# Kernel tuning notes

Hardware: AMD Instinct MI355X
Metric: run time of the kernel (lower is better)

The kernel has to match this reference:

```python
import jax, jax.numpy as jnp
import numpy as np

B, D = 64, 512          # batch, in_dims
P, PS, S = 128, 3, 64   # num_patches, patch_size, scene_size


def setup_inputs() -> dict:
    key = jax.random.key(0)
    k0, k1, k2, k3 = jax.random.split(key, 4)
    z = jax.random.normal(k0, (B, D), jnp.float32)
    Wm = jax.random.normal(k1, (P * PS * PS, D), jnp.float32) * 0.02
    bm = jnp.zeros((P * PS * PS,), jnp.float32)
    Wt = jax.random.normal(k2, (6 * P, D), jnp.float32) * 0.01
    # module initializes transform bias to [scale,0,0,0,scale,0] per patch (scale=2)
    bt = jnp.tile(jnp.array([2.0, 0.0, 0.0, 0.0, 2.0, 0.0], jnp.float32), P)
    noise = jax.random.normal(k3, (PS, PS), jnp.float32)
    return {"z": z, "Wm": Wm, "bm": bm, "Wt": Wt, "bt": bt, "noise": noise}


def _affine_grid(theta, size):
    # theta: (N,2,3). Matches torch affine_grid(align_corners=False).
    c = (jnp.arange(size, dtype=theta.dtype) + 0.5) / size * 2.0 - 1.0
    xg, yg = jnp.meshgrid(c, c)  # xg[h,w]=c[w], yg[h,w]=c[h]
    base = jnp.stack([xg, yg, jnp.ones_like(xg)], axis=-1)  # (S,S,3)
    return jnp.einsum('nij,hwj->nhwi', theta, base)  # (N,S,S,2), [...,0]=x, [...,1]=y


def _grid_sample_bilinear_zeros(img, grid):
    # img: (N,Hi,Wi), grid: (N,Ho,Wo,2). torch grid_sample bilinear, zeros padding,
    # align_corners=False.
    N, Hi, Wi = img.shape
    ix = ((grid[..., 0] + 1.0) * Wi - 1.0) * 0.5
    iy = ((grid[..., 1] + 1.0) * Hi - 1.0) * 0.5
    ix0 = jnp.floor(ix)
    iy0 = jnp.floor(iy)
    wx1 = ix - ix0
    wy1 = iy - iy0
    wx0 = 1.0 - wx1
    wy0 = 1.0 - wy1
    b = jnp.arange(N)[:, None, None]

    def gather(xf, yf):
        xi = xf.astype(jnp.int32)
        yi = yf.astype(jnp.int32)
        valid = (xi >= 0) & (xi < Wi) & (yi >= 0) & (yi < Hi)
        xc = jnp.clip(xi, 0, Wi - 1)
        yc = jnp.clip(yi, 0, Hi - 1)
        return jnp.where(valid, img[b, yc, xc], 0.0)

    v00 = gather(ix0, iy0)
    v01 = gather(ix0 + 1.0, iy0)
    v10 = gather(ix0, iy0 + 1.0)
    v11 = gather(ix0 + 1.0, iy0 + 1.0)
    return (wy0 * (wx0 * v00 + wx1 * v01) + wy1 * (wx0 * v10 + wx1 * v11))


def reference(z, Wm, bm, Wt, bt, noise):
    Bz = z.shape[0]
    # refine_patches=True path: masks = 1 - sigmoid(Linear(z))
    masks = 1.0 - jax.nn.sigmoid(z @ Wm.T + bm)
    masks = masks.reshape(Bz, P, PS, PS) * noise  # patch_noise multiply
    theta = (z @ Wt.T + bt).reshape(Bz, P, 2, 3)
    imgs = masks.reshape(Bz * P, PS, PS)
    th = theta.reshape(Bz * P, 2, 3)
    grid = _affine_grid(th, S)                      # (B*P, S, S, 2)
    out = _grid_sample_bilinear_zeros(imgs, grid)   # (B*P, S, S)
    return out.reshape(Bz, P, S, S)
```

## Files before the change

### kernel.cpp

```cpp
#include <hip/hip_runtime.h>
#include <math.h>

#define BATCH 64
#define DIM 512
#define NPATCH 128
#define SSZ 64
#define PADZ 516

typedef float f32x4 __attribute__((ext_vector_type(4)));

__global__ __launch_bounds__(256) void k_gemm(
    const float* __restrict__ z, const float* __restrict__ Wm,
    const float* __restrict__ bm, const float* __restrict__ Wt,
    const float* __restrict__ bt, const float* __restrict__ noise,
    float* __restrict__ ws) {
  __shared__ float zs[16 * PADZ];
  const int p = blockIdx.x;
  const int bq = blockIdx.y;
  const int t = threadIdx.x;

  {
    const f32x4* __restrict__ src = (const f32x4*)(z + (size_t)(bq * 16) * DIM);
#pragma unroll
    for (int i = 0; i < 8; ++i) {
      const int idx = t + (i << 8);
      const int row = idx >> 7;
      const int col = idx & 127;
      *(f32x4*)(zs + row * PADZ + (col << 2)) = src[idx];
    }
  }
  __syncthreads();

  const int r = t >> 4;
  const int bl = t & 15;
  if (r >= 15) return;

  const float* __restrict__ wrow =
      (r < 9) ? (Wm + (size_t)(p * 9 + r) * DIM)
              : (Wt + (size_t)(p * 6 + (r - 9)) * DIM);
  const float* __restrict__ zr = zs + bl * PADZ;

  float a0 = 0.0f, a1 = 0.0f, a2 = 0.0f, a3 = 0.0f;
#pragma unroll 8
  for (int i = 0; i < 128; ++i) {
    const f32x4 wv = ((const f32x4*)wrow)[i];
    const f32x4 zv = *(const f32x4*)(zr + (i << 2));
    a0 = fmaf(wv.x, zv.x, a0);
    a1 = fmaf(wv.y, zv.y, a1);
    a2 = fmaf(wv.z, zv.z, a2);
    a3 = fmaf(wv.w, zv.w, a3);
  }
  const float acc = (a0 + a1) + (a2 + a3);

  const int b = (bq << 4) + bl;
  float v;
  if (r < 9) {
    v = (1.0f / (1.0f + expf(acc + bm[p * 9 + r]))) * noise[r];
  } else {
    v = acc + bt[p * 6 + (r - 9)];
  }
  ws[(((size_t)b << 7) + p) * 16 + r] = v;
}

__global__ __launch_bounds__(256) void k_sample(
    const float* __restrict__ ws, float* __restrict__ out) {
  __shared__ float sm[16];
  const int t = threadIdx.x;
  const int bp = blockIdx.x;
  if (t < 16) sm[t] = ws[((size_t)bp << 4) + t];
  __syncthreads();

  const float m00 = sm[0], m01 = sm[1], m02 = sm[2];
  const float m10 = sm[3], m11 = sm[4], m12 = sm[5];
  const float m20 = sm[6], m21 = sm[7], m22 = sm[8];
  const float th0 = sm[9], th1 = sm[10], th2 = sm[11];
  const float th3 = sm[12], th4 = sm[13], th5 = sm[14];

  const int w4 = (t & 15) << 2;
  const int hb = t >> 4;
  const float cx0 = (w4 + 0.5f) * (1.0f / 32.0f) - 1.0f;
  const float cy0 = (hb + 0.5f) * (1.0f / 32.0f) - 1.0f;
  const float dix = th0 * (1.5f / 32.0f);
  const float diy = th3 * (1.5f / 32.0f);
  const float Bx = 1.5f * th1, By = 1.5f * th4;
  const float Px = fmaf(1.5f, fmaf(th0, cx0, th2), 1.0f);
  const float Py = fmaf(1.5f, fmaf(th3, cx0, th5), 1.0f);

  float* op = out + ((size_t)bp << 12) + hb * 64 + w4;

#pragma unroll
  for (int i = 0; i < 4; ++i) {
    const float cy = cy0 + 0.5f * i;
    const float ix = fmaf(Bx, cy, Px);
    const float iy = fmaf(By, cy, Py);
    float ax = ix + 1.0f, bx = 1.0f - ix;
    float ay = iy + 1.0f, by = 1.0f - iy;
    f32x4 rv;
#pragma unroll
    for (int j = 0; j < 4; ++j) {
      const float wx0 = __builtin_amdgcn_fmed3f(0.0f, ax, bx);
      const float wx1 = __builtin_amdgcn_fmed3f(0.0f, ax - 1.0f, bx + 1.0f);
      const float wx2 = __builtin_amdgcn_fmed3f(0.0f, ax - 2.0f, bx + 2.0f);
      const float wy0 = __builtin_amdgcn_fmed3f(0.0f, ay, by);
      const float wy1 = __builtin_amdgcn_fmed3f(0.0f, ay - 1.0f, by + 1.0f);
      const float wy2 = __builtin_amdgcn_fmed3f(0.0f, ay - 2.0f, by + 2.0f);
      const float s0 = fmaf(m02, wx2, fmaf(m01, wx1, m00 * wx0));
      const float s1 = fmaf(m12, wx2, fmaf(m11, wx1, m10 * wx0));
      const float s2 = fmaf(m22, wx2, fmaf(m21, wx1, m20 * wx0));
      rv[j] = fmaf(wy2, s2, fmaf(wy1, s1, wy0 * s0));
      ax += dix; bx -= dix;
      ay += diy; by -= diy;
    }
    __builtin_nontemporal_store(rv, (f32x4*)(op + i * 16 * 64));
  }
}

__global__ __launch_bounds__(256) void k_fused(
    const float* __restrict__ z, const float* __restrict__ Wm,
    const float* __restrict__ bm, const float* __restrict__ Wt,
    const float* __restrict__ bt, const float* __restrict__ noise,
    float* __restrict__ out) {
  __shared__ float sm[16];

  const int t = threadIdx.x;
  const int bp = blockIdx.x;
  const int b = bp >> 7;
  const int p = bp & 127;

  const int r = t >> 4;
  const int c = t & 15;
  float acc = 0.0f;
  if (r < 15) {
    const float* __restrict__ wrow =
        (r < 9) ? (Wm + (size_t)(p * 9 + r) * DIM)
                : (Wt + (size_t)(p * 6 + (r - 9)) * DIM);
    const float* __restrict__ zrow = z + (size_t)b * DIM;
#pragma unroll
    for (int i = 0; i < 8; ++i) {
      const float4 wv = *(const float4*)(wrow + i * 64 + c * 4);
      const float4 zv = *(const float4*)(zrow + i * 64 + c * 4);
      acc = fmaf(wv.x, zv.x, acc);
      acc = fmaf(wv.y, zv.y, acc);
      acc = fmaf(wv.z, zv.z, acc);
      acc = fmaf(wv.w, zv.w, acc);
    }
  }
  acc += __shfl_xor(acc, 1);
  acc += __shfl_xor(acc, 2);
  acc += __shfl_xor(acc, 4);
  acc += __shfl_xor(acc, 8);
  if (c == 0 && r < 15) {
    float v = acc;
    if (r < 9) {
      v = (1.0f / (1.0f + expf(v + bm[p * 9 + r]))) * noise[r];
    } else {
      v += bt[p * 6 + (r - 9)];
    }
    sm[r] = v;
  }
  __syncthreads();

  const float m00 = sm[0], m01 = sm[1], m02 = sm[2];
  const float m10 = sm[3], m11 = sm[4], m12 = sm[5];
  const float m20 = sm[6], m21 = sm[7], m22 = sm[8];
  const float th0 = sm[9], th1 = sm[10], th2 = sm[11];
  const float th3 = sm[12], th4 = sm[13], th5 = sm[14];

  const int w4 = (t & 15) << 2;
  const int hb = t >> 4;
  const float cx0 = (w4 + 0.5f) * (1.0f / 32.0f) - 1.0f;
  const float cy0 = (hb + 0.5f) * (1.0f / 32.0f) - 1.0f;
  const float dix = th0 * (1.5f / 32.0f);
  const float diy = th3 * (1.5f / 32.0f);
  const float Bx = 1.5f * th1, By = 1.5f * th4;
  const float Px = fmaf(1.5f, fmaf(th0, cx0, th2), 1.0f);
  const float Py = fmaf(1.5f, fmaf(th3, cx0, th5), 1.0f);

  float* op = out + ((size_t)bp << 12) + hb * 64 + w4;

#pragma unroll
  for (int i = 0; i < 4; ++i) {
    const float cy = cy0 + 0.5f * i;
    float ix = fmaf(Bx, cy, Px);
    float iy = fmaf(By, cy, Py);
    float4 rv;
    float* rp = &rv.x;
#pragma unroll
    for (int j = 0; j < 4; ++j) {
      const float wx0 = fmaxf(1.0f - fabsf(ix), 0.0f);
      const float wx1 = fmaxf(1.0f - fabsf(ix - 1.0f), 0.0f);
      const float wx2 = fmaxf(1.0f - fabsf(ix - 2.0f), 0.0f);
      const float wy0 = fmaxf(1.0f - fabsf(iy), 0.0f);
      const float wy1 = fmaxf(1.0f - fabsf(iy - 1.0f), 0.0f);
      const float wy2 = fmaxf(1.0f - fabsf(iy - 2.0f), 0.0f);
      const float s0 = fmaf(m02, wx2, fmaf(m01, wx1, m00 * wx0));
      const float s1 = fmaf(m12, wx2, fmaf(m11, wx1, m10 * wx0));
      const float s2 = fmaf(m22, wx2, fmaf(m21, wx1, m20 * wx0));
      rp[j] = fmaf(wy2, s2, fmaf(wy1, s1, wy0 * s0));
      ix += dix;
      iy += diy;
    }
    *(float4*)(op + i * 16 * 64) = rv;
  }
}

extern "C" void kernel_launch(void* const* d_in, const int* in_sizes, int n_in,
                              void* d_out, int out_size, void* d_ws, size_t ws_size,
                              hipStream_t stream) {
  const float* z     = (const float*)d_in[0];
  const float* Wm    = (const float*)d_in[1];
  const float* bm    = (const float*)d_in[2];
  const float* Wt    = (const float*)d_in[3];
  const float* bt    = (const float*)d_in[4];
  const float* noise = (const float*)d_in[5];
  float* out = (float*)d_out;

  const size_t need = (size_t)BATCH * NPATCH * 16 * sizeof(float);
  if (d_ws != nullptr && ws_size >= need) {
    float* ws = (float*)d_ws;
    hipLaunchKernelGGL(k_gemm, dim3(NPATCH, 4), dim3(256), 0, stream,
                       z, Wm, bm, Wt, bt, noise, ws);
    hipLaunchKernelGGL(k_sample, dim3(BATCH * NPATCH), dim3(256), 0, stream,
                       ws, out);
  } else {
    hipLaunchKernelGGL(k_fused, dim3(BATCH * NPATCH), dim3(256), 0, stream,
                       z, Wm, bm, Wt, bt, noise, out);
  }
}
```

Measured before the change: 162.4 us.

## Assign one wavefront per patch in sampling kernel, broadcast params via shuffles

The sampling kernel now gives each 64-lane wavefront a whole 64x64 patch, so a 256-thread block covers four patches and the grid shrinks fourfold. Per-patch parameters are loaded by one lane each and broadcast with wave shuffles instead of going through shared memory and a block barrier. Each lane loops over 16 row groups and writes float4s with ordinary stores in place of nontemporal ones. This removes the shared-memory staging and __syncthreads, at the cost of more serial work per thread and a change in output caching behaviour.

```diff
diff --git a/kernel.cpp b/kernel.cpp
--- a/kernel.cpp
+++ b/kernel.cpp
@@ -64,40 +64,38 @@
 
 __global__ __launch_bounds__(256) void k_sample(
     const float* __restrict__ ws, float* __restrict__ out) {
-  __shared__ float sm[16];
-  const int t = threadIdx.x;
-  const int bp = blockIdx.x;
-  if (t < 16) sm[t] = ws[((size_t)bp << 4) + t];
-  __syncthreads();
-
-  const float m00 = sm[0], m01 = sm[1], m02 = sm[2];
-  const float m10 = sm[3], m11 = sm[4], m12 = sm[5];
-  const float m20 = sm[6], m21 = sm[7], m22 = sm[8];
-  const float th0 = sm[9], th1 = sm[10], th2 = sm[11];
-  const float th3 = sm[12], th4 = sm[13], th5 = sm[14];
-
-  const int w4 = (t & 15) << 2;
-  const int hb = t >> 4;
+  const int lane = threadIdx.x & 63;
+  const int bp = (blockIdx.x << 2) | (threadIdx.x >> 6);
+
+  const float rec = ws[((size_t)bp << 4) + (lane & 15)];
+  const float m00 = __shfl(rec, 0), m01 = __shfl(rec, 1), m02 = __shfl(rec, 2);
+  const float m10 = __shfl(rec, 3), m11 = __shfl(rec, 4), m12 = __shfl(rec, 5);
+  const float m20 = __shfl(rec, 6), m21 = __shfl(rec, 7), m22 = __shfl(rec, 8);
+  const float th0 = __shfl(rec, 9), th1 = __shfl(rec, 10), th2 = __shfl(rec, 11);
+  const float th3 = __shfl(rec, 12), th4 = __shfl(rec, 13), th5 = __shfl(rec, 14);
+
+  const int w4 = (lane & 15) << 2;
+  const int rsub = lane >> 4;
   const float cx0 = (w4 + 0.5f) * (1.0f / 32.0f) - 1.0f;
-  const float cy0 = (hb + 0.5f) * (1.0f / 32.0f) - 1.0f;
+  const float cy0 = (rsub + 0.5f) * (1.0f / 32.0f) - 1.0f;
   const float dix = th0 * (1.5f / 32.0f);
   const float diy = th3 * (1.5f / 32.0f);
-  const float Bx = 1.5f * th1, By = 1.5f * th4;
-  const float Px = fmaf(1.5f, fmaf(th0, cx0, th2), 1.0f);
-  const float Py = fmaf(1.5f, fmaf(th3, cx0, th5), 1.0f);
-
-  float* op = out + ((size_t)bp << 12) + hb * 64 + w4;
-
-#pragma unroll
-  for (int i = 0; i < 4; ++i) {
-    const float cy = cy0 + 0.5f * i;
-    const float ix = fmaf(Bx, cy, Px);
-    const float iy = fmaf(By, cy, Py);
-    float ax = ix + 1.0f, bx = 1.0f - ix;
-    float ay = iy + 1.0f, by = 1.0f - iy;
+  const float dAx = th1 * (1.5f * 0.125f);
+  const float dAy = th4 * (1.5f * 0.125f);
+  const float ixb0 = fmaf(1.5f, fmaf(th0, cx0, fmaf(th1, cy0, th2)), 1.0f);
+  const float iyb0 = fmaf(1.5f, fmaf(th3, cx0, fmaf(th4, cy0, th5)), 1.0f);
+
+  float* op = out + ((size_t)bp << 12) + (rsub << 6) + w4;
+
+#pragma unroll 2
+  for (int a = 0; a < 16; ++a) {
+    float ix = fmaf((float)a, dAx, ixb0);
+    float iy = fmaf((float)a, dAy, iyb0);
     f32x4 rv;
 #pragma unroll
     for (int j = 0; j < 4; ++j) {
+      const float ax = ix + 1.0f, bx = 1.0f - ix;
+      const float ay = iy + 1.0f, by = 1.0f - iy;
       const float wx0 = __builtin_amdgcn_fmed3f(0.0f, ax, bx);
       const float wx1 = __builtin_amdgcn_fmed3f(0.0f, ax - 1.0f, bx + 1.0f);
       const float wx2 = __builtin_amdgcn_fmed3f(0.0f, ax - 2.0f, bx + 2.0f);
@@ -108,10 +106,11 @@
       const float s1 = fmaf(m12, wx2, fmaf(m11, wx1, m10 * wx0));
       const float s2 = fmaf(m22, wx2, fmaf(m21, wx1, m20 * wx0));
       rv[j] = fmaf(wy2, s2, fmaf(wy1, s1, wy0 * s0));
-      ax += dix; bx -= dix;
-      ay += diy; by -= diy;
-    }
-    __builtin_nontemporal_store(rv, (f32x4*)(op + i * 16 * 64));
+      ix += dix;
+      iy += diy;
+    }
+    *(f32x4*)op = rv;
+    op += 256;
   }
 }
 
@@ -220,7 +219,7 @@
     float* ws = (float*)d_ws;
     hipLaunchKernelGGL(k_gemm, dim3(NPATCH, 4), dim3(256), 0, stream,
                        z, Wm, bm, Wt, bt, noise, ws);
-    hipLaunchKernelGGL(k_sample, dim3(BATCH * NPATCH), dim3(256), 0, stream,
+    hipLaunchKernelGGL(k_sample, dim3(BATCH * NPATCH / 4), dim3(256), 0, stream,
                        ws, out);
   } else {
     hipLaunchKernelGGL(k_fused, dim3(BATCH * NPATCH), dim3(256), 0, stream,
```

New measurement: 159.7 us. Within noise of the previous version (-1.7%).
